# Kernel optimization log

Measured on AMD Instinct MI355X. Metric: run time of the kernel, lower is better.

## Reference

```python
import jax, jax.numpy as jnp
import numpy as np

D_MODEL = 1024
N_HEADS = 16
HEAD_DIM = D_MODEL // N_HEADS
B, S = 2, 2048


def setup_inputs() -> dict:
    key = jax.random.key(0)
    ks = jax.random.split(key, 6)
    w_scale = 1.0 / np.sqrt(D_MODEL)
    return {
        "query": jax.random.normal(ks[0], (B, S, D_MODEL), dtype=jnp.float32),
        "Wq": jax.random.normal(ks[1], (D_MODEL, D_MODEL), dtype=jnp.float32) * w_scale,
        "Wk": jax.random.normal(ks[2], (D_MODEL, D_MODEL), dtype=jnp.float32) * w_scale,
        "Wv": jax.random.normal(ks[3], (D_MODEL, D_MODEL), dtype=jnp.float32) * w_scale,
        "Wo": jax.random.normal(ks[4], (D_MODEL, D_MODEL), dtype=jnp.float32) * w_scale,
        "bo": jnp.zeros((D_MODEL,), dtype=jnp.float32),
    }


def reference(query, Wq, Wk, Wv, Wo, bo):
    # Self-attention: key = value = query (forward() defaults).
    b, t, _ = query.shape
    # Q/K/V projections (nn.Linear applies x @ W.T; weights here are stored as
    # [out, in] like torch, so project with W.T). Split into heads: [B,H,T,Dh].
    def proj(x, W):
        return (x @ W.T).reshape(b, t, N_HEADS, HEAD_DIM).transpose(0, 2, 1, 3)

    q = proj(query, Wq)
    k = proj(query, Wk)
    v = proj(query, Wv)

    scale = 1.0 / np.sqrt(HEAD_DIM)
    scores = jnp.einsum("bhqd,bhkd->bhqk", q, k) * scale  # [B,H,T,T]
    # Causal mask (is_causal=True, not cross-attention).
    causal = jnp.tril(jnp.ones((t, t), dtype=bool))
    scores = jnp.where(causal, scores, jnp.finfo(scores.dtype).min)
    weights = jax.nn.softmax(scores, axis=-1)
    out = jnp.einsum("bhqk,bhkd->bhqd", weights, v)  # [B,H,T,Dh]
    out = out.transpose(0, 2, 1, 3).reshape(b, t, D_MODEL)
    # Output projection with bias (dropout is identity in eval mode).
    return out @ Wo.T + bo
```

## Files before the change

### kernel.cpp

```cpp
#include <hip/hip_runtime.h>
#include <hip/hip_bf16.h>
#include <math.h>

typedef __attribute__((ext_vector_type(8))) short short8;
typedef __attribute__((ext_vector_type(4))) float floatx4;
typedef __attribute__((ext_vector_type(2))) _Float16 half2v;
typedef __attribute__((ext_vector_type(4))) _Float16 half4v;

#define MFMA_BF16_32(a, b, c) __builtin_amdgcn_mfma_f32_16x16x32_bf16(a, b, c, 0, 0, 0)
#define MFMA_F16_16(a, b, c) __builtin_amdgcn_mfma_f32_16x16x16f16(a, b, c, 0, 0, 0)

#define PIPE_BAR2() asm volatile("s_waitcnt vmcnt(2)\n\ts_barrier" ::: "memory")
#define PIPE_BAR0() asm volatile("s_waitcnt vmcnt(0)\n\ts_barrier" ::: "memory")
#define GEMM_BAR4() asm volatile("s_waitcnt vmcnt(4) lgkmcnt(0)\n\ts_barrier" ::: "memory")
#define GEMM_BAR3() asm volatile("s_waitcnt vmcnt(3) lgkmcnt(0)\n\ts_barrier" ::: "memory")
#define GEMM_BAR0() asm volatile("s_waitcnt vmcnt(0) lgkmcnt(0)\n\ts_barrier" ::: "memory")

static constexpr int NH = 16;
static constexpr int Bb = 2;
static constexpr int Ss = 2048;
static constexpr int DM = 1024;

__device__ inline unsigned short f2bf(float f) {
    unsigned int u = __float_as_uint(f);
    u += 0x7fffu + ((u >> 16) & 1u);
    return (unsigned short)(u >> 16);
}

__device__ __forceinline__ half2v pkrtz(float a, float b) {
    return __builtin_bit_cast(half2v, __builtin_amdgcn_cvt_pkrtz(a, b));
}

__device__ __forceinline__ void gload_lds16(const unsigned short* g, unsigned short* l) {
    __builtin_amdgcn_global_load_lds(
        (const __attribute__((address_space(1))) unsigned int*)g,
        (__attribute__((address_space(3))) unsigned int*)l, 16, 0, 0);
}

__global__ void convert_all(const float* __restrict__ X, const float* __restrict__ w0,
                            const float* __restrict__ w1, const float* __restrict__ w2,
                            const float* __restrict__ w3, unsigned short* __restrict__ dstX,
                            unsigned short* __restrict__ dstW) {
    const int bid = blockIdx.x;
    const float* src;
    unsigned short* dst;
    int i;
    if (bid < 4096) {
        src = X; dst = dstX; i = bid * 256 + threadIdx.x;
    } else {
        const int w = (bid - 4096) >> 10;
        src = (w == 0) ? w0 : (w == 1) ? w1 : (w == 2) ? w2 : w3;
        dst = dstW + (size_t)w * 1048576;
        i = ((bid - 4096) & 1023) * 256 + threadIdx.x;
    }
    float4 v = ((const float4*)src)[i];
    ushort4 o;
    o.x = f2bf(v.x); o.y = f2bf(v.y); o.z = f2bf(v.z); o.w = f2bf(v.w);
    ((ushort4*)dst)[i] = o;
}

__global__ __launch_bounds__(256, 3) void gemm_qkv(const unsigned short* __restrict__ A,
                                                   const unsigned short* __restrict__ W,
                                                   unsigned short* __restrict__ Qp,
                                                   unsigned short* __restrict__ Kp,
                                                   unsigned short* __restrict__ Vt) {
    __shared__ __align__(16) unsigned short S[3][8192];
    const int K = 1024;
    const int tid = threadIdx.x;
    const int wave = tid >> 6, lane = tid & 63;
    const int quad = lane >> 4, l16 = lane & 15;
    const int wr = wave >> 1, wc = wave & 1;

    const int lin = blockIdx.x;
    const int xcd = lin & 7, slot = lin >> 3;
    const int bxt = (xcd & 3) * 8 + (slot & 7);
    const int by = (xcd >> 2) * 12 + (slot >> 3);
    const int bm = bxt * 128;
    const int bn = by * 128;

    const int srow = tid >> 2;
    const int scg = (tid & 3) ^ ((srow >> 1) & 3);
    const unsigned short* gA0 = A + (size_t)(bm + srow) * K + scg * 8;
    const unsigned short* gB0 = W + (size_t)(bn + srow) * K + scg * 8;

    auto stage = [&](int k0, int buf) {
        gload_lds16(gA0 + k0, &S[buf][wave * 512]);
        gload_lds16(gA0 + (size_t)64 * K + k0, &S[buf][2048 + wave * 512]);
        gload_lds16(gB0 + k0, &S[buf][4096 + wave * 512]);
        gload_lds16(gB0 + (size_t)64 * K + k0, &S[buf][6144 + wave * 512]);
    };

    floatx4 acc[4][4];
#pragma unroll
    for (int i = 0; i < 4; i++)
#pragma unroll
        for (int j = 0; j < 4; j++) acc[i][j] = (floatx4)0.0f;

    stage(0, 0);
    stage(32, 1);
    int buf = 0;
    for (int k0 = 0; k0 < K; k0 += 32) {
        if (k0 + 32 < K) { GEMM_BAR4(); } else { GEMM_BAR0(); }
        const int nbuf = (buf == 2) ? 0 : buf + 1;
        const int pbuf = (nbuf == 2) ? 0 : nbuf + 1;
        if (k0 + 64 < K) stage(k0 + 64, pbuf);
        short8 af[4];
#pragma unroll
        for (int im = 0; im < 4; im++) {
            const int frow = wr * 64 + im * 16 + l16;
            af[im] = *(const short8*)&S[buf][frow * 32 + ((quad ^ ((frow >> 1) & 3)) * 8)];
        }
#pragma unroll
        for (int jn = 0; jn < 4; jn++) {
            const int frow = wc * 64 + jn * 16 + l16;
            short8 bf = *(const short8*)&S[buf][4096 + frow * 32 +
                                               ((quad ^ ((frow >> 1) & 3)) * 8)];
#pragma unroll
            for (int im = 0; im < 4; im++) acc[im][jn] = MFMA_BF16_32(af[im], bf, acc[im][jn]);
        }
        buf = nbuf;
    }
    __syncthreads();

    if (by < 16) {
        unsigned short* LB = &S[0][0];
        unsigned short* dst = (by < 8) ? Qp : Kp;
        const int nb = (by & 7) * 128;
        const float scale = (by < 8) ? 0.125f : 1.0f;
#pragma unroll
        for (int im = 0; im < 4; im++)
#pragma unroll
            for (int jn = 0; jn < 4; jn++) {
                const int row = wr * 64 + im * 16 + quad * 4;
                const int col = wc * 64 + jn * 16 + l16;
#pragma unroll
                for (int r = 0; r < 4; r++)
                    LB[(row + r) * 132 + col] = f2bf(acc[im][jn][r] * scale);
            }
        __syncthreads();
#pragma unroll
        for (int i = 0; i < 8; ++i) {
            const int flat = i * 256 + tid;
            const int row = flat >> 4, ch = flat & 15;
            short8 v = *(const short8*)&LB[row * 132 + ch * 8];
            *(short8*)&dst[(size_t)(bm + row) * 1024 + nb + ch * 8] = v;
        }
    } else {
        _Float16* LF = (_Float16*)&S[0][0];
        const int dbase = (by - 16) * 128;
        const int bI = bm >> 11, sbase = bm & 2047;
#pragma unroll
        for (int im = 0; im < 4; im++)
#pragma unroll
            for (int jn = 0; jn < 4; jn++) {
                const int d = wc * 64 + jn * 16 + l16;
                const int sl = wr * 64 + im * 16 + quad * 4;
                *(half2v*)&LF[d * 130 + sl] = pkrtz(acc[im][jn][0], acc[im][jn][1]);
                *(half2v*)&LF[d * 130 + sl + 2] = pkrtz(acc[im][jn][2], acc[im][jn][3]);
            }
        __syncthreads();
#pragma unroll
        for (int i = 0; i < 8; ++i) {
            const int flat = i * 256 + tid;
            const int dr = flat >> 4, ch = flat & 15;
            short8 v = *(const short8*)&LF[dr * 130 + ch * 8];
            const int d = dbase + dr;
            const int head = d >> 6, d64 = d & 63;
            *(short8*)&Vt[(((size_t)(bI * 16 + head)) * 64 + d64) * 2048 + sbase + ch * 8] = v;
        }
    }
}

__global__ __launch_bounds__(256, 4) void gemm_out(const unsigned short* __restrict__ A,
                                                   const unsigned short* __restrict__ Bm,
                                                   float* __restrict__ C,
                                                   const float* __restrict__ bias) {
    __shared__ __align__(16) unsigned short As[3][4096];
    __shared__ __align__(16) unsigned short Bs[3][2048];
    const int K = 1024;
    const int tid = threadIdx.x;
    const int wave = tid >> 6, lane = tid & 63;
    const int quad = lane >> 4, l16 = lane & 15;

    const int l = blockIdx.x;
    const int xcd = l & 7, slot = l >> 3;
    const int bx = (xcd & 3) * 8 + (slot & 7);
    const int by = (xcd >> 2) * 8 + (slot >> 3);
    const int bm = bx * 128, bn = by * 64;

    const int srow = tid >> 2;
    const int scg = (tid & 3) ^ ((srow >> 1) & 3);
    const unsigned short* gA0 = A + (size_t)(bm + srow) * K + scg * 8;
    const unsigned short* gB0 = Bm + (size_t)(bn + srow) * K + scg * 8;

    auto stage = [&](int k0, int buf) {
        gload_lds16(gA0 + k0, &As[buf][wave * 512]);
        gload_lds16(gA0 + (size_t)64 * K + k0, &As[buf][2048 + wave * 512]);
        gload_lds16(gB0 + k0, &Bs[buf][wave * 512]);
    };

    floatx4 acc[2][4];
#pragma unroll
    for (int i = 0; i < 2; i++)
#pragma unroll
        for (int j = 0; j < 4; j++) acc[i][j] = (floatx4)0.0f;

    stage(0, 0);
    stage(32, 1);
    int buf = 0;
    for (int k0 = 0; k0 < K; k0 += 32) {
        if (k0 + 32 < K) { GEMM_BAR3(); } else { GEMM_BAR0(); }
        const int nbuf = (buf == 2) ? 0 : buf + 1;
        const int pbuf = (nbuf == 2) ? 0 : nbuf + 1;
        if (k0 + 64 < K) stage(k0 + 64, pbuf);
        short8 af[2];
#pragma unroll
        for (int im = 0; im < 2; im++) {
            const int frow = wave * 32 + im * 16 + l16;
            af[im] = *(const short8*)&As[buf][frow * 32 + ((quad ^ ((frow >> 1) & 3)) * 8)];
        }
#pragma unroll
        for (int jn = 0; jn < 4; jn++) {
            const int frow = jn * 16 + l16;
            short8 bf = *(const short8*)&Bs[buf][frow * 32 + ((quad ^ ((frow >> 1) & 3)) * 8)];
#pragma unroll
            for (int im = 0; im < 2; im++) acc[im][jn] = MFMA_BF16_32(af[im], bf, acc[im][jn]);
        }
        buf = nbuf;
    }

#pragma unroll
    for (int im = 0; im < 2; im++) {
#pragma unroll
        for (int jn = 0; jn < 4; jn++) {
            const int row0 = bm + wave * 32 + im * 16 + quad * 4;
            const int colg = bn + jn * 16 + l16;
            const float bv = bias[colg];
#pragma unroll
            for (int r = 0; r < 4; r++)
                C[(size_t)(row0 + r) * 1024 + colg] = acc[im][jn][r] + bv;
        }
    }
}

__global__ __launch_bounds__(512, 4) void flash_attn(const unsigned short* __restrict__ Qp,
                                                     const unsigned short* __restrict__ Kp,
                                                     const _Float16* __restrict__ Vt,
                                                     unsigned short* __restrict__ Out) {
    __shared__ __align__(16) unsigned short Ks[3][4096];
    __shared__ __align__(16) _Float16 Vs[3][4096];
    const int lin = blockIdx.x;
    const int xcd = lin & 7, slot = lin >> 3;
    const int pair = xcd * 4 + ((slot >> 4) & 3);
    const int h = pair & 15, b = pair >> 4;
    const int qt0 = slot & 15;
    const int qt = ((slot >> 5) & 1) ? 15 - qt0 : qt0;

    const int tid = threadIdx.x, w = tid >> 6, lane = tid & 63;
    const int quad = lane >> 4, l16 = lane & 15;

    short8 qf[2];
    {
        const unsigned short* qa =
            Qp + ((size_t)(b * 2048 + qt * 128 + w * 16 + l16) << 10) + h * 64 + quad * 8;
        qf[0] = *(const short8*)qa;
        qf[1] = *(const short8*)(qa + 32);
    }

    const int t8 = tid >> 3;
    const int cg = (tid & 7) ^ (t8 & 7);
    const unsigned short* gK0 = Kp + ((size_t)(b * 2048 + t8) << 10) + h * 64 + cg * 8;
    const _Float16* gV0 = Vt + ((size_t)((b * 16 + h) * 64 + t8) << 11) + cg * 8;
    unsigned short* ldsK = &Ks[0][0] + w * 512;
    _Float16* ldsV = &Vs[0][0] + w * 512;

    auto stage = [&](int kt, int buf) {
        const size_t ko = (size_t)kt << 16;
        const size_t vo = (size_t)kt << 6;
        gload_lds16(gK0 + ko, ldsK + buf * 4096);
        gload_lds16((const unsigned short*)(gV0 + vo), (unsigned short*)(ldsV + buf * 4096));
    };

    const int ktEnd = 2 * qt + 1;
    const int myEnd = 2 * qt + (w >> 2);
    stage(0, 0);
    stage(1, 1);

    floatx4 acc[4];
#pragma unroll
    for (int dt = 0; dt < 4; dt++) acc[dt] = (floatx4)0.0f;
    float lsum = 0.0f;
    const int qloc = (w & 3) * 16 + l16;
    const int sw = l16 & 7;

    int buf = 0;
    for (int kt = 0; kt <= ktEnd; ++kt) {
        if (kt < ktEnd) { PIPE_BAR2(); } else { PIPE_BAR0(); }
        const int nbuf = (buf == 2) ? 0 : buf + 1;
        const int pbuf = (nbuf == 2) ? 0 : nbuf + 1;
        if (kt + 2 <= ktEnd) stage(kt + 2, pbuf);
        if (kt <= myEnd) {
            const bool diag = (kt == myEnd);
            const int scMax = diag ? (w & 3) : 3;
            const unsigned short* KB = &Ks[buf][0];
            const _Float16* VB = &Vs[buf][0];

#pragma unroll
            for (int sc = 0; sc < 4; ++sc) {
                if (sc <= scMax) {
                    const int rowk = sc * 16 + l16;
                    short8 kf0 = *(const short8*)&KB[rowk * 64 + ((quad ^ sw) * 8)];
                    short8 kf1 = *(const short8*)&KB[rowk * 64 + (((4 + quad) ^ sw) * 8)];

                    floatx4 s = MFMA_BF16_32(kf0, qf[0], (floatx4)(-2.0f));
                    s = MFMA_BF16_32(kf1, qf[1], s);
                    float ps[4];
#pragma unroll
                    for (int r = 0; r < 4; ++r) {
                        float e = __expf(s[r]);
                        if (diag && (sc * 16 + quad * 4 + r > qloc)) e = 0.0f;
                        ps[r] = e;
                    }
                    lsum += (ps[0] + ps[1]) + (ps[2] + ps[3]);
                    half4v p = __builtin_shufflevector(pkrtz(ps[0], ps[1]),
                                                       pkrtz(ps[2], ps[3]), 0, 1, 2, 3);

#pragma unroll
                    for (int dt = 0; dt < 4; ++dt) {
                        const int rowv = dt * 16 + l16;
                        const int cgv = ((sc * 2 + (quad >> 1)) ^ sw);
                        half4v vf = *(const half4v*)&VB[rowv * 64 + cgv * 8 + (quad & 1) * 4];
                        acc[dt] = MFMA_F16_16(vf, p, acc[dt]);
                    }
                }
            }
        }
        buf = nbuf;
    }

    lsum += __shfl_xor(lsum, 16);
    lsum += __shfl_xor(lsum, 32);
    const float inv = 1.0f / lsum;

    const size_t row = (size_t)(b * 2048 + qt * 128 + w * 16 + l16);
#pragma unroll
    for (int dt = 0; dt < 4; ++dt) {
        const int col = h * 64 + dt * 16 + quad * 4;
        ushort4 o;
        o.x = f2bf(acc[dt][0] * inv);
        o.y = f2bf(acc[dt][1] * inv);
        o.z = f2bf(acc[dt][2] * inv);
        o.w = f2bf(acc[dt][3] * inv);
        *(ushort4*)&Out[row * 1024 + col] = o;
    }
}

extern "C" void kernel_launch(void* const* d_in, const int* in_sizes, int n_in,
                              void* d_out, int out_size, void* d_ws, size_t ws_size,
                              hipStream_t stream) {
    const float* X  = (const float*)d_in[0];
    const float* Wq = (const float*)d_in[1];
    const float* Wk = (const float*)d_in[2];
    const float* Wv = (const float*)d_in[3];
    const float* Wo = (const float*)d_in[4];
    const float* bo = (const float*)d_in[5];

    unsigned short* ws = (unsigned short*)d_ws;
    unsigned short* Xb   = ws;
    unsigned short* W4   = ws + (size_t)4194304;
    unsigned short* Wob  = W4 + (size_t)3145728;
    unsigned short* Qp   = ws + (size_t)8388608;
    unsigned short* Kp   = ws + (size_t)12582912;
    unsigned short* Vt   = ws + (size_t)16777216;
    unsigned short* At   = ws + (size_t)20971520;

    convert_all<<<8192, 256, 0, stream>>>(X, Wq, Wk, Wv, Wo, Xb, W4);

    gemm_qkv<<<768, 256, 0, stream>>>(Xb, W4, Qp, Kp, Vt);

    flash_attn<<<512, 512, 0, stream>>>(Qp, Kp, (const _Float16*)Vt, At);

    gemm_out<<<512, 256, 0, stream>>>(At, Wob, (float*)d_out, bo);
}
```

Before: 178.4 us.

## Split KV range across two wave groups with LDS reduction in flash attention

The flash attention block is reorganised so two groups of four waves each process half of the key/value tiles. Each wave now handles two 16-row query slices (rows A and B), so every loaded K/V fragment feeds twice the MFMA work. The two partial accumulators and row sums are combined through LDS at the end. Pipelining changes from a triple buffer per block to a double buffer per group with a mid-loop barrier. This aims to raise MFMA reuse per LDS read and balance causal work, at the cost of more registers (launch bounds lowered to 2), an extra LDS reduction, and an added barrier per step.

```diff
diff --git a/kernel.cpp b/kernel.cpp
--- a/kernel.cpp
+++ b/kernel.cpp
@@ -10,8 +10,9 @@
 #define MFMA_BF16_32(a, b, c) __builtin_amdgcn_mfma_f32_16x16x32_bf16(a, b, c, 0, 0, 0)
 #define MFMA_F16_16(a, b, c) __builtin_amdgcn_mfma_f32_16x16x16f16(a, b, c, 0, 0, 0)
 
-#define PIPE_BAR2() asm volatile("s_waitcnt vmcnt(2)\n\ts_barrier" ::: "memory")
-#define PIPE_BAR0() asm volatile("s_waitcnt vmcnt(0)\n\ts_barrier" ::: "memory")
+#define FA_BAR4() asm volatile("s_waitcnt vmcnt(4)\n\ts_barrier" ::: "memory")
+#define FA_BAR0() asm volatile("s_waitcnt vmcnt(0)\n\ts_barrier" ::: "memory")
+#define FA_MID()  asm volatile("s_waitcnt lgkmcnt(0)\n\ts_barrier" ::: "memory")
 #define GEMM_BAR4() asm volatile("s_waitcnt vmcnt(4) lgkmcnt(0)\n\ts_barrier" ::: "memory")
 #define GEMM_BAR3() asm volatile("s_waitcnt vmcnt(3) lgkmcnt(0)\n\ts_barrier" ::: "memory")
 #define GEMM_BAR0() asm volatile("s_waitcnt vmcnt(0) lgkmcnt(0)\n\ts_barrier" ::: "memory")
@@ -243,12 +244,11 @@
     }
 }
 
-__global__ __launch_bounds__(512, 4) void flash_attn(const unsigned short* __restrict__ Qp,
+__global__ __launch_bounds__(512, 2) void flash_attn(const unsigned short* __restrict__ Qp,
                                                      const unsigned short* __restrict__ Kp,
                                                      const _Float16* __restrict__ Vt,
                                                      unsigned short* __restrict__ Out) {
-    __shared__ __align__(16) unsigned short Ks[3][4096];
-    __shared__ __align__(16) _Float16 Vs[3][4096];
+    __shared__ __align__(16) unsigned short SMEM[32768];
     const int lin = blockIdx.x;
     const int xcd = lin & 7, slot = lin >> 3;
     const int pair = xcd * 4 + ((slot >> 4) & 3);
@@ -257,101 +257,147 @@
     const int qt = ((slot >> 5) & 1) ? 15 - qt0 : qt0;
 
     const int tid = threadIdx.x, w = tid >> 6, lane = tid & 63;
+    const int g = w >> 2, wg = w & 3;
     const int quad = lane >> 4, l16 = lane & 15;
 
-    short8 qf[2];
+    short8 qfA[2], qfB[2];
     {
         const unsigned short* qa =
-            Qp + ((size_t)(b * 2048 + qt * 128 + w * 16 + l16) << 10) + h * 64 + quad * 8;
-        qf[0] = *(const short8*)qa;
-        qf[1] = *(const short8*)(qa + 32);
-    }
-
-    const int t8 = tid >> 3;
-    const int cg = (tid & 7) ^ (t8 & 7);
+            Qp + ((size_t)(b * 2048 + qt * 128 + wg * 16 + l16) << 10) + h * 64 + quad * 8;
+        qfA[0] = *(const short8*)qa;
+        qfA[1] = *(const short8*)(qa + 32);
+        const unsigned short* qb = qa + ((size_t)64 << 10);
+        qfB[0] = *(const short8*)qb;
+        qfB[1] = *(const short8*)(qb + 32);
+    }
+
+    const int lt = tid & 255;
+    const int t8 = lt >> 3;
+    const int cg = (lt & 7) ^ (t8 & 7);
     const unsigned short* gK0 = Kp + ((size_t)(b * 2048 + t8) << 10) + h * 64 + cg * 8;
+    const unsigned short* gK1 = gK0 + ((size_t)32 << 10);
     const _Float16* gV0 = Vt + ((size_t)((b * 16 + h) * 64 + t8) << 11) + cg * 8;
-    unsigned short* ldsK = &Ks[0][0] + w * 512;
-    _Float16* ldsV = &Vs[0][0] + w * 512;
+    const _Float16* gV1 = gV0 + ((size_t)32 << 11);
+    unsigned short* KSb = SMEM + g * 8192;
+    _Float16* VSb = (_Float16*)(SMEM + 16384) + g * 8192;
+    unsigned short* ldsK = KSb + wg * 512;
+    _Float16* ldsV = VSb + wg * 512;
 
     auto stage = [&](int kt, int buf) {
         const size_t ko = (size_t)kt << 16;
         const size_t vo = (size_t)kt << 6;
         gload_lds16(gK0 + ko, ldsK + buf * 4096);
+        gload_lds16(gK1 + ko, ldsK + buf * 4096 + 2048);
         gload_lds16((const unsigned short*)(gV0 + vo), (unsigned short*)(ldsV + buf * 4096));
+        gload_lds16((const unsigned short*)(gV1 + vo), (unsigned short*)(ldsV + buf * 4096 + 2048));
     };
 
-    const int ktEnd = 2 * qt + 1;
-    const int myEnd = 2 * qt + (w >> 2);
-    stage(0, 0);
-    stage(1, 1);
-
-    floatx4 acc[4];
-#pragma unroll
-    for (int dt = 0; dt < 4; dt++) acc[dt] = (floatx4)0.0f;
-    float lsum = 0.0f;
-    const int qloc = (w & 3) * 16 + l16;
+    const int steps = qt + 1;
+    const int ktBase = g * steps;
+    stage(ktBase, 0);
+    if (steps > 1) stage(ktBase + 1, 1);
+
+    floatx4 accA[4], accB[4];
+#pragma unroll
+    for (int dt = 0; dt < 4; dt++) { accA[dt] = (floatx4)0.0f; accB[dt] = (floatx4)0.0f; }
+    float lA = 0.0f, lB = 0.0f;
+    const int qloc = wg * 16 + l16;
     const int sw = l16 & 7;
 
-    int buf = 0;
-    for (int kt = 0; kt <= ktEnd; ++kt) {
-        if (kt < ktEnd) { PIPE_BAR2(); } else { PIPE_BAR0(); }
-        const int nbuf = (buf == 2) ? 0 : buf + 1;
-        const int pbuf = (nbuf == 2) ? 0 : nbuf + 1;
-        if (kt + 2 <= ktEnd) stage(kt + 2, pbuf);
-        if (kt <= myEnd) {
-            const bool diag = (kt == myEnd);
-            const int scMax = diag ? (w & 3) : 3;
-            const unsigned short* KB = &Ks[buf][0];
-            const _Float16* VB = &Vs[buf][0];
-
-#pragma unroll
-            for (int sc = 0; sc < 4; ++sc) {
-                if (sc <= scMax) {
-                    const int rowk = sc * 16 + l16;
-                    short8 kf0 = *(const short8*)&KB[rowk * 64 + ((quad ^ sw) * 8)];
-                    short8 kf1 = *(const short8*)&KB[rowk * 64 + (((4 + quad) ^ sw) * 8)];
-
-                    floatx4 s = MFMA_BF16_32(kf0, qf[0], (floatx4)(-2.0f));
-                    s = MFMA_BF16_32(kf1, qf[1], s);
-                    float ps[4];
-#pragma unroll
-                    for (int r = 0; r < 4; ++r) {
-                        float e = __expf(s[r]);
-                        if (diag && (sc * 16 + quad * 4 + r > qloc)) e = 0.0f;
-                        ps[r] = e;
-                    }
-                    lsum += (ps[0] + ps[1]) + (ps[2] + ps[3]);
-                    half4v p = __builtin_shufflevector(pkrtz(ps[0], ps[1]),
-                                                       pkrtz(ps[2], ps[3]), 0, 1, 2, 3);
-
-#pragma unroll
-                    for (int dt = 0; dt < 4; ++dt) {
-                        const int rowv = dt * 16 + l16;
-                        const int cgv = ((sc * 2 + (quad >> 1)) ^ sw);
-                        half4v vf = *(const half4v*)&VB[rowv * 64 + cgv * 8 + (quad & 1) * 4];
-                        acc[dt] = MFMA_F16_16(vf, p, acc[dt]);
-                    }
+    for (int t = 0; t < steps; ++t) {
+        const int kt = ktBase + t;
+        if (t + 1 < steps) { FA_BAR4(); } else { FA_BAR0(); }
+        const bool aAct = (kt <= 2 * qt);
+        const bool aDiag = (kt == 2 * qt);
+        const bool bDiag = (kt == 2 * qt + 1);
+        const unsigned short* KB = KSb + (t & 1) * 4096;
+        const _Float16* VB = VSb + (t & 1) * 4096;
+
+#pragma unroll
+        for (int sc = 0; sc < 4; ++sc) {
+            const int rowk = sc * 16 + l16;
+            short8 kf0 = *(const short8*)&KB[rowk * 64 + ((quad ^ sw) * 8)];
+            short8 kf1 = *(const short8*)&KB[rowk * 64 + (((4 + quad) ^ sw) * 8)];
+
+            half4v pA, pB;
+            if (aAct) {
+                floatx4 sA = MFMA_BF16_32(kf0, qfA[0], (floatx4)(-2.0f));
+                sA = MFMA_BF16_32(kf1, qfA[1], sA);
+                float ps[4];
+#pragma unroll
+                for (int r = 0; r < 4; ++r) {
+                    float e = __expf(sA[r]);
+                    if (aDiag && (sc * 16 + quad * 4 + r > qloc)) e = 0.0f;
+                    ps[r] = e;
                 }
+                lA += (ps[0] + ps[1]) + (ps[2] + ps[3]);
+                pA = __builtin_shufflevector(pkrtz(ps[0], ps[1]), pkrtz(ps[2], ps[3]), 0, 1, 2, 3);
             }
-        }
-        buf = nbuf;
-    }
-
-    lsum += __shfl_xor(lsum, 16);
-    lsum += __shfl_xor(lsum, 32);
-    const float inv = 1.0f / lsum;
-
-    const size_t row = (size_t)(b * 2048 + qt * 128 + w * 16 + l16);
-#pragma unroll
-    for (int dt = 0; dt < 4; ++dt) {
-        const int col = h * 64 + dt * 16 + quad * 4;
-        ushort4 o;
-        o.x = f2bf(acc[dt][0] * inv);
-        o.y = f2bf(acc[dt][1] * inv);
-        o.z = f2bf(acc[dt][2] * inv);
-        o.w = f2bf(acc[dt][3] * inv);
-        *(ushort4*)&Out[row * 1024 + col] = o;
+            {
+                floatx4 sB = MFMA_BF16_32(kf0, qfB[0], (floatx4)(-2.0f));
+                sB = MFMA_BF16_32(kf1, qfB[1], sB);
+                float ps[4];
+#pragma unroll
+                for (int r = 0; r < 4; ++r) {
+                    float e = __expf(sB[r]);
+                    if (bDiag && (sc * 16 + quad * 4 + r > qloc)) e = 0.0f;
+                    ps[r] = e;
+                }
+                lB += (ps[0] + ps[1]) + (ps[2] + ps[3]);
+                pB = __builtin_shufflevector(pkrtz(ps[0], ps[1]), pkrtz(ps[2], ps[3]), 0, 1, 2, 3);
+            }
+
+#pragma unroll
+            for (int dt = 0; dt < 4; ++dt) {
+                const int rowv = dt * 16 + l16;
+                const int cgv = ((sc * 2 + (quad >> 1)) ^ sw);
+                half4v vf = *(const half4v*)&VB[rowv * 64 + cgv * 8 + (quad & 1) * 4];
+                if (aAct) accA[dt] = MFMA_F16_16(vf, pA, accA[dt]);
+                accB[dt] = MFMA_F16_16(vf, pB, accB[dt]);
+            }
+        }
+        FA_MID();
+        if (t + 2 < steps) stage(ktBase + t + 2, t & 1);
+    }
+
+    lA += __shfl_xor(lA, 16); lA += __shfl_xor(lA, 32);
+    lB += __shfl_xor(lB, 16); lB += __shfl_xor(lB, 32);
+
+    float* F = (float*)SMEM;
+    if (g == 1) {
+        float* dstf = F + (wg * 64 + lane) * 36;
+#pragma unroll
+        for (int dt = 0; dt < 4; ++dt) {
+            *(floatx4*)(dstf + dt * 4) = accA[dt];
+            *(floatx4*)(dstf + 16 + dt * 4) = accB[dt];
+        }
+        dstf[32] = lA; dstf[33] = lB;
+    }
+    __syncthreads();
+    if (g == 0) {
+        const float* srcf = F + (wg * 64 + lane) * 36;
+#pragma unroll
+        for (int dt = 0; dt < 4; ++dt) {
+            accA[dt] += *(const floatx4*)(srcf + dt * 4);
+            accB[dt] += *(const floatx4*)(srcf + 16 + dt * 4);
+        }
+        lA += srcf[32]; lB += srcf[33];
+        const float iA = 1.0f / lA;
+        const float iB = 1.0f / lB;
+
+        const size_t rowA = (size_t)(b * 2048 + qt * 128 + wg * 16 + l16);
+        const size_t rowB = rowA + 64;
+#pragma unroll
+        for (int dt = 0; dt < 4; ++dt) {
+            const int col = h * 64 + dt * 16 + quad * 4;
+            ushort4 oa, ob;
+            oa.x = f2bf(accA[dt][0] * iA); oa.y = f2bf(accA[dt][1] * iA);
+            oa.z = f2bf(accA[dt][2] * iA); oa.w = f2bf(accA[dt][3] * iA);
+            ob.x = f2bf(accB[dt][0] * iB); ob.y = f2bf(accB[dt][1] * iB);
+            ob.z = f2bf(accB[dt][2] * iB); ob.w = f2bf(accB[dt][3] * iB);
+            *(ushort4*)&Out[rowA * 1024 + col] = oa;
+            *(ushort4*)&Out[rowB * 1024 + col] = ob;
+        }
     }
 }
 
```

New measurement: 218.5 us. +22.4%, slower.
